# Kernel tuning notes

Measured on AMD Instinct MI355X. Metric: run time of the kernel, lower is better.

Reference implementation:

```python
import jax, jax.numpy as jnp
import numpy as np

IMG_W, IMG_H = 960.0, 512.0   # image_size (w, h)
HM_W, HM_H = 240, 128         # heatmap_size (w, h)


def _bilinear(fmap, gx, gy):
    # fmap: [C,H,W]; gx, gy: [N] normalized coords; bilinear, align_corners=False, zero padding
    C, H, W = fmap.shape
    ix = (gx + 1.0) * W * 0.5 - 0.5
    iy = (gy + 1.0) * H * 0.5 - 0.5
    x0f = jnp.floor(ix); y0f = jnp.floor(iy)
    wx1 = ix - x0f; wy1 = iy - y0f

    def tap(xf, yf, wgt):
        valid = (xf >= 0) & (xf <= W - 1) & (yf >= 0) & (yf <= H - 1)
        xc = jnp.clip(xf.astype(jnp.int32), 0, W - 1)
        yc = jnp.clip(yf.astype(jnp.int32), 0, H - 1)
        return fmap[:, yc, xc] * (wgt * valid.astype(fmap.dtype))

    return (tap(x0f, y0f, (1 - wx1) * (1 - wy1)) + tap(x0f + 1, y0f, wx1 * (1 - wy1))
            + tap(x0f, y0f + 1, (1 - wx1) * wy1) + tap(x0f + 1, y0f + 1, wx1 * wy1))


def _forward(feature_maps, grid_center, space_center, space_size, sub_space_size,
             cube, centers, trans, cam_R, cam_T, cam_f, cam_c):
    n_cam, B, C, H, W = feature_maps.shape
    vox = jnp.float32(cube)
    fine_n = (space_size / sub_space_size * (vox - 1.0)).astype(jnp.int32) + 1   # [3]
    fine_nf = fine_n.astype(jnp.float32)
    scale = (fine_nf - 1.0) / space_size
    bias = (-sub_space_size / 2.0 / space_size * (fine_nf - 1.0)
            - scale * (space_center - space_size / 2.0))
    centers_tl = jnp.round(grid_center[:, :3] * scale + bias).astype(jnp.int32)  # [B,3]
    offset = (centers_tl.astype(jnp.float32) / (fine_nf - 1.0) * space_size
              - space_size / 2.0 + sub_space_size / 2.0)                          # [B,3]
    mask_xy = jnp.maximum(((1.0 - grid_center[:, 5:7]) / 2.0 * (vox - 1.0)).astype(jnp.int32), 0)
    mask = jnp.concatenate([mask_xy, jnp.zeros((B, 1), jnp.int32)], axis=1)       # [B,3]
    start = jnp.maximum(centers_tl + mask, 0)
    end = jnp.minimum(centers_tl + cube - mask, fine_n)
    end = jnp.maximum(end, start + 1)

    # fixed-size sub-cube of fine-grid indices; out-of-window cells are masked to 0
    v = jnp.arange(cube)
    mesh = jnp.stack(jnp.meshgrid(v, v, v, indexing="ij"), axis=-1).reshape(-1, 3)  # [N,3]
    fidx = centers_tl[:, None, :] + mesh[None]                                       # [B,N,3]
    valid = jnp.all((fidx >= start[:, None, :]) & (fidx < end[:, None, :]), axis=-1)  # [B,N]
    valid = valid & (grid_center[:, 3:4] >= 0)
    world = (space_center - space_size / 2.0
             + fidx.astype(jnp.float32) / (fine_nf - 1.0) * space_size)              # [B,N,3]

    # pinhole world->pixel per (batch, camera)
    rel = world[:, None, :, :] - cam_T[:, :, None, :]                                # [B,K,N,3]
    Xc = jnp.einsum("bkij,bknj->bkni", cam_R, rel)
    xy = cam_f[:, :, None, :] * Xc[..., :2] / Xc[..., 2:3] + cam_c[:, :, None, :]    # [B,K,N,2]
    maxwh = jnp.max(centers * 2.0, axis=-1)[:, :, None, None]
    xy = jnp.clip(xy, -1.0, maxwh)
    xy = jnp.einsum("bkij,bknj->bkni", trans[..., :2], xy) + trans[:, :, None, :, 2]  # affine crop
    xy = xy * jnp.array([HM_W / IMG_W, HM_H / IMG_H], jnp.float32)
    g = jnp.clip(xy / jnp.array([HM_W - 1.0, HM_H - 1.0], jnp.float32) * 2.0 - 1.0, -1.1, 1.1)

    fm = jnp.transpose(feature_maps, (1, 0, 2, 3, 4))                                # [B,K,C,H,W]
    samp = jax.vmap(jax.vmap(_bilinear))(fm, g[..., 0], g[..., 1])                   # [B,K,C,N]
    samp = samp * valid[:, None, None, :].astype(samp.dtype)
    cubes = jnp.sum(samp, axis=1) / (n_cam + 1e-6)            # mean agg (bounding==1)
    cubes = jnp.clip(cubes, 0.0, 1.0).reshape(B, C, cube, cube, cube)
    return cubes, offset


def setup_inputs() -> dict:
    key = jax.random.key(0)
    ks = jax.random.split(key, 10)
    n_cam, B, C, H, W = 5, 4, 15, 128, 240
    feature_maps = jax.random.uniform(ks[0], (n_cam, B, C, H, W), jnp.float32)
    xy = jax.random.uniform(ks[1], (B, 2), minval=-3000.0, maxval=3000.0)
    z = jax.random.uniform(ks[2], (B, 1), minval=800.0, maxval=1200.0)
    flag = jnp.ones((B, 2), jnp.float32)  # cols 3 (validity >= 0) and 4
    m = jax.random.uniform(ks[3], (B, 2), minval=0.6, maxval=1.0)  # cols 5:7 mask fracs
    grid_center = jnp.concatenate([xy, z, flag, m], axis=1)        # [B,7]
    space_center = jnp.array([0.0, 0.0, 1000.0], jnp.float32)
    space_size = jnp.array([8000.0, 8000.0, 2000.0], jnp.float32)
    sub_space_size = jnp.array([2000.0, 2000.0, 2000.0], jnp.float32)
    centers = jnp.array([IMG_W / 2, IMG_H / 2], jnp.float32) + \
        jax.random.uniform(ks[4], (B, n_cam, 2), minval=-5.0, maxval=5.0)
    base = jnp.array([[1.0, 0.0, 0.0], [0.0, 1.0, 0.0]], jnp.float32)
    trans = base + 0.01 * jax.random.normal(ks[5], (B, n_cam, 2, 3), jnp.float32)
    cam_R = jnp.eye(3, dtype=jnp.float32) + 0.05 * jax.random.normal(ks[6], (B, n_cam, 3, 3), jnp.float32)
    t_xy = jax.random.uniform(ks[7], (B, n_cam, 2), minval=-500.0, maxval=500.0)
    cam_T = jnp.concatenate([t_xy, jnp.full((B, n_cam, 1), -6000.0, jnp.float32)], axis=-1)
    cam_f = jax.random.uniform(ks[8], (B, n_cam, 2), minval=500.0, maxval=700.0)
    cam_c = jnp.array([IMG_W / 2, IMG_H / 2], jnp.float32) + \
        jax.random.uniform(ks[9], (B, n_cam, 2), minval=-10.0, maxval=10.0)
    return {"feature_maps": feature_maps, "grid_center": grid_center,
            "space_center": space_center, "space_size": space_size,
            "sub_space_size": sub_space_size, "sub_cube_size": 64,
            "centers": centers, "trans": trans, "cam_R": cam_R,
            "cam_T": cam_T, "cam_f": cam_f, "cam_c": cam_c}


def reference(feature_maps, grid_center, space_center, space_size, sub_space_size,
              sub_cube_size, centers, trans, cam_R, cam_T, cam_f, cam_c):
    return _forward(feature_maps, grid_center, space_center, space_size, sub_space_size,
                    int(sub_cube_size), centers, trans, cam_R, cam_T, cam_f, cam_c)
```

## Files before the change

### kernel.cpp

```cpp
#include <hip/hip_runtime.h>
#include <hip/hip_fp16.h>

#define NCAM 5
#define NC 15
#define NCP 16
#define FH 128
#define FW 240
#define HW (FH*FW)
#define CUBE 64
#define NVOX (CUBE*CUBE*CUBE)
#define TTHREADS 256
#define MTHREADS 256
#define CSTR 24

__global__ __launch_bounds__(TTHREADS) void transpose_fm(
    const float* __restrict__ fm, __half* __restrict__ fmH,
    const float* __restrict__ gc, const float* __restrict__ space_c,
    const float* __restrict__ space_s, const float* __restrict__ sub_s,
    const float* __restrict__ centers, const float* __restrict__ trans,
    const float* __restrict__ cam_R, const float* __restrict__ cam_T,
    const float* __restrict__ cam_f, const float* __restrict__ cam_c,
    float* __restrict__ camS, int* __restrict__ bwin,
    float* __restrict__ out, int B)
{
    const int t = threadIdx.x;
    const int cb = blockIdx.y;
    const int cam = cb / B, b = cb - cam * B;
    const int bk = b * NCAM + cam;

    if (blockIdx.x == 0 && blockIdx.y == 0) {
        if (t < B) {
            const int bb = t;
            #pragma unroll
            for (int d = 0; d < 3; ++d) {
                float ssz = space_s[d], sc = space_c[d], sub = sub_s[d];
                int   fn  = (int)(ssz / sub * (CUBE - 1.0f)) + 1;
                float fnf = (float)fn;
                float scale = (fnf - 1.0f) / ssz;
                float bias  = -sub / 2.0f / ssz * (fnf - 1.0f) - scale * (sc - ssz / 2.0f);
                int ctl = (int)rintf(gc[bb*7 + d] * scale + bias);
                int mask = 0;
                if (d < 2) {
                    mask = (int)((1.0f - gc[bb*7 + 5 + d]) / 2.0f * (CUBE - 1.0f));
                    if (mask < 0) mask = 0;
                }
                int st = max(ctl + mask, 0);
                int en = min(ctl + CUBE - mask, fn);
                en = max(en, st + 1);
                bwin[bb*12 + d]     = ctl;
                bwin[bb*12 + 3 + d] = st;
                bwin[bb*12 + 6 + d] = en;
                out[(size_t)B * NC * NVOX + bb*3 + d] =
                    (float)ctl / (fnf - 1.0f) * ssz - ssz / 2.0f + sub / 2.0f;
            }
            bwin[t*12 + 9] = (gc[t*7 + 3] >= 0.0f) ? 1 : 0;
        }
        if (t < B * NCAM) {
            const int k = t;
            float sA[3], bA[3];
            #pragma unroll
            for (int d = 0; d < 3; ++d) {
                float ssz = space_s[d], sub = sub_s[d];
                int   fn  = (int)(ssz / sub * (CUBE - 1.0f)) + 1;
                sA[d] = ssz / ((float)fn - 1.0f);
                bA[d] = space_c[d] - ssz * 0.5f;
            }
            const float* R = cam_R + k*9;
            const float* T = cam_T + k*3;
            float* P = camS + (size_t)k * CSTR;
            #pragma unroll
            for (int i = 0; i < 3; ++i) {
                #pragma unroll
                for (int d = 0; d < 3; ++d) P[i*3 + d] = R[i*3 + d] * sA[d];
                P[9 + i] = R[i*3+0]*(bA[0]-T[0]) + R[i*3+1]*(bA[1]-T[1]) + R[i*3+2]*(bA[2]-T[2]);
            }
            P[12] = cam_f[k*2+0];  P[13] = cam_f[k*2+1];
            P[14] = cam_c[k*2+0];  P[15] = cam_c[k*2+1];
            P[16] = fmaxf(centers[k*2+0]*2.0f, centers[k*2+1]*2.0f);
            const float* tr = trans + k*6;
            const float KX = 60.0f/239.0f, KY = 32.0f/127.0f;
            P[17] = tr[0]*KX;  P[18] = tr[1]*KX;  P[19] = tr[2]*KX - 120.0f;
            P[20] = tr[3]*KY;  P[21] = tr[4]*KY;  P[22] = tr[5]*KY - 64.0f;
            P[23] = 0.0f;
        }
    }

    float sA[3], bA[3];
    #pragma unroll
    for (int d = 0; d < 3; ++d) {
        float ssz = space_s[d], sub = sub_s[d];
        int fn = (int)(ssz / sub * (CUBE - 1.0f)) + 1;
        sA[d] = ssz / ((float)fn - 1.0f);
        bA[d] = space_c[d] - ssz * 0.5f;
    }
    const float* R = cam_R + bk*9;
    const float* T = cam_T + bk*3;
    float M[9], tv[3];
    #pragma unroll
    for (int i = 0; i < 3; ++i) {
        #pragma unroll
        for (int d = 0; d < 3; ++d) M[i*3+d] = R[i*3+d] * sA[d];
        tv[i] = R[i*3+0]*(bA[0]-T[0]) + R[i*3+1]*(bA[1]-T[1]) + R[i*3+2]*(bA[2]-T[2]);
    }
    const float f0 = cam_f[bk*2+0], f1 = cam_f[bk*2+1];
    const float c0 = cam_c[bk*2+0], c1 = cam_c[bk*2+1];
    const float mw = fmaxf(centers[bk*2+0]*2.0f, centers[bk*2+1]*2.0f);
    const float* tr = trans + bk*6;
    const float KX = 60.0f/239.0f, KY = 32.0f/127.0f;
    const float ax = tr[0]*KX, bx_ = tr[1]*KX, cxo = tr[2]*KX - 120.0f;
    const float ay = tr[3]*KY, by_ = tr[4]*KY, cyo = tr[5]*KY - 64.0f;

    float ctlf[3];
    #pragma unroll
    for (int d = 0; d < 3; ++d) {
        float ssz = space_s[d], sc = space_c[d], sub = sub_s[d];
        int fn = (int)(ssz / sub * (CUBE - 1.0f)) + 1;
        float fnf = (float)fn;
        float scale = (fnf - 1.0f) / ssz;
        float bias = -sub/2.0f/ssz*(fnf-1.0f) - scale*(sc - ssz/2.0f);
        ctlf[d] = rintf(gc[b*7+d]*scale + bias);
    }

    float pxmin = 1e30f, pxmax = -1e30f, pymin = 1e30f, pymax = -1e30f;
    bool ok = true;
    #pragma unroll
    for (int ci = 0; ci < 8; ++ci) {
        float vx = ctlf[0] + ((ci & 1) ? 63.0f : 0.0f);
        float vy = ctlf[1] + ((ci & 2) ? 63.0f : 0.0f);
        float vz = ctlf[2] + ((ci & 4) ? 63.0f : 0.0f);
        float X0 = fmaf(M[0],vx, fmaf(M[1],vy, fmaf(M[2],vz, tv[0])));
        float X1 = fmaf(M[3],vx, fmaf(M[4],vy, fmaf(M[5],vz, tv[1])));
        float X2 = fmaf(M[6],vx, fmaf(M[7],vy, fmaf(M[8],vz, tv[2])));
        ok = ok && (X2 > 1e-3f);
        float rz = __builtin_amdgcn_rcpf(X2);
        float px = fmaf(f0*X0, rz, c0);
        float py = fmaf(f1*X1, rz, c1);
        pxmin = fminf(pxmin, px); pxmax = fmaxf(pxmax, px);
        pymin = fminf(pymin, py); pymax = fmaxf(pymax, py);
    }
    int bbx0, bbx1, bby0, bby1;
    if (ok) {
        float pxl = fminf(fmaxf(pxmin,-1.0f),mw), pxh = fminf(fmaxf(pxmax,-1.0f),mw);
        float pyl = fminf(fmaxf(pymin,-1.0f),mw), pyh = fminf(fmaxf(pymax,-1.0f),mw);
        float ixlo = (ax>0.f?ax*pxl:ax*pxh) + (bx_>0.f?bx_*pyl:bx_*pyh) + cxo;
        float ixhi = (ax>0.f?ax*pxh:ax*pxl) + (bx_>0.f?bx_*pyh:bx_*pyl) + cxo;
        ixlo = fminf(fmaxf(ixlo,-132.0f),132.0f) + 119.5f;
        ixhi = fminf(fmaxf(ixhi,-132.0f),132.0f) + 119.5f;
        float iylo = (ay>0.f?ay*pxl:ay*pxh) + (by_>0.f?by_*pyl:by_*pyh) + cyo;
        float iyhi = (ay>0.f?ay*pxh:ay*pxl) + (by_>0.f?by_*pyh:by_*pyl) + cyo;
        iylo = fminf(fmaxf(iylo,-70.4f),70.4f) + 63.5f;
        iyhi = fminf(fmaxf(iyhi,-70.4f),70.4f) + 63.5f;
        bbx0 = max((int)floorf(ixlo) - 1, 0);
        bbx1 = min((int)floorf(ixhi) + 2, FW-1);
        bby0 = max((int)floorf(iylo) - 1, 0);
        bby1 = min((int)floorf(iyhi) + 2, FH-1);
    } else {
        bbx0 = 0; bbx1 = FW-1; bby0 = 0; bby1 = FH-1;
    }

    const int p0  = blockIdx.x * TTHREADS;
    const int rlo = p0 / FW, rhi = (p0 + TTHREADS - 1) / FW;
    if (rhi < bby0 || rlo > bby1) return;
    const int p   = p0 + t;
    const int pyy = p / FW, pxx = p - pyy * FW;
    if (pyy < bby0 || pyy > bby1 || pxx < bbx0 || pxx > bbx1) return;

    const float* src = fm + (size_t)cb * NC * HW + p;
    __half v[NCP];
    #pragma unroll
    for (int c = 0; c < NC; ++c) v[c] = __float2half(src[(size_t)c * HW]);
    v[15] = __float2half(0.0f);
    uint4* dst = (uint4*)(fmH + ((size_t)cb * HW + p) * NCP);
    dst[0] = *(const uint4*)(v);
    dst[1] = *(const uint4*)(v + 8);
}

__device__ __forceinline__ __half2 u2h(unsigned u) {
    __half2 h; __builtin_memcpy(&h, &u, 4); return h;
}

#define TAPFMA2(W2, A, Bv)                                                    \
    acc2[0] = __hfma2((W2), u2h(A.x),  acc2[0]);                              \
    acc2[1] = __hfma2((W2), u2h(A.y),  acc2[1]);                              \
    acc2[2] = __hfma2((W2), u2h(A.z),  acc2[2]);                              \
    acc2[3] = __hfma2((W2), u2h(A.w),  acc2[3]);                              \
    acc2[4] = __hfma2((W2), u2h(Bv.x), acc2[4]);                              \
    acc2[5] = __hfma2((W2), u2h(Bv.y), acc2[5]);                              \
    acc2[6] = __hfma2((W2), u2h(Bv.z), acc2[6]);                              \
    acc2[7] = __hfma2((W2), u2h(Bv.w), acc2[7]);

__global__ __launch_bounds__(MTHREADS) void proj_main(
    const __half* __restrict__ fmH,
    const float* __restrict__ camS,
    const int* __restrict__ bwin,
    float* __restrict__ out, int B)
{
    const unsigned nwg = gridDim.x;
    const unsigned q = nwg >> 3, r = nwg & 7;
    const unsigned xcd = blockIdx.x & 7, idx = blockIdx.x >> 3;
    const unsigned wgid = (xcd < r ? xcd * (q + 1) : r * (q + 1) + (xcd - r) * q) + idx;

    const int b = wgid >> 10;
    const int n = (int)(wgid & 1023) * MTHREADS + threadIdx.x;
    const int vi = n >> 12, vj = (n >> 6) & 63, vk = n & 63;

    const int* W = bwin + b*12;
    const int fx = W[0] + vi, fy = W[1] + vj, fz = W[2] + vk;
    const bool valid = (fx >= W[3]) & (fx < W[6])
                     & (fy >= W[4]) & (fy < W[7])
                     & (fz >= W[5]) & (fz < W[8])
                     & (W[9] != 0);

    __half2 acc2[8];
    #pragma unroll
    for (int i = 0; i < 8; ++i) acc2[i] = __half2half2(__float2half(0.0f));

    if (valid) {
        const float fxf = (float)fx, fyf = (float)fy, fzf = (float)fz;
        const float* cs = camS + (size_t)(b * NCAM) * CSTR;

        #pragma unroll
        for (int cam = 0; cam < NCAM; ++cam) {
            const float* P = cs + cam * CSTR;
            float X0 = fmaf(P[0], fxf, fmaf(P[1], fyf, fmaf(P[2], fzf, P[9])));
            float X1 = fmaf(P[3], fxf, fmaf(P[4], fyf, fmaf(P[5], fzf, P[10])));
            float X2 = fmaf(P[6], fxf, fmaf(P[7], fyf, fmaf(P[8], fzf, P[11])));
            float rz = __builtin_amdgcn_rcpf(X2);
            float px = fmaf(P[12]*X0, rz, P[14]);
            float py = fmaf(P[13]*X1, rz, P[15]);
            float mw = P[16];
            px = fminf(fmaxf(px, -1.0f), mw);
            py = fminf(fmaxf(py, -1.0f), mw);
            float ixf = fminf(fmaxf(fmaf(P[17], px, fmaf(P[18], py, P[19])), -132.0f), 132.0f) + 119.5f;
            float iyf = fminf(fmaxf(fmaf(P[20], px, fmaf(P[21], py, P[22])), -70.4f), 70.4f) + 63.5f;
            float x0f = floorf(ixf), y0f = floorf(iyf);
            float wx1 = ixf - x0f,  wy1 = iyf - y0f;
            float wx0 = 1.0f - wx1, wy0 = 1.0f - wy1;
            int x0 = (int)x0f, y0 = (int)y0f, x1 = x0 + 1, y1 = y0 + 1;
            bool vx0 = (unsigned)x0 <= (FW-1), vx1 = (unsigned)x1 <= (FW-1);
            bool vy0 = (unsigned)y0 <= (FH-1), vy1 = (unsigned)y1 <= (FH-1);
            float w0 = (vx0 && vy0) ? wx0*wy0 : 0.0f;
            float w1 = (vx1 && vy0) ? wx1*wy0 : 0.0f;
            float w2 = (vx0 && vy1) ? wx0*wy1 : 0.0f;
            float w3 = (vx1 && vy1) ? wx1*wy1 : 0.0f;
            int xc0 = min(max(x0,0),FW-1), xc1 = min(max(x1,0),FW-1);
            int yc0 = min(max(y0,0),FH-1), yc1 = min(max(y1,0),FH-1);

            const __half* bp  = fmH + (size_t)(cam*B + b) * HW * NCP;
            const __half* t00 = bp  + (size_t)(yc0*FW + xc0) * NCP;
            const __half* t10 = t00 + (size_t)(xc1 - xc0) * NCP;
            const __half* t01 = t00 + (size_t)(yc1 - yc0) * (FW * NCP);
            const __half* t11 = t01 + (size_t)(xc1 - xc0) * NCP;

            uint4 a0 = ((const uint4*)t00)[0], b0 = ((const uint4*)t00)[1];
            uint4 a1 = ((const uint4*)t10)[0], b1 = ((const uint4*)t10)[1];
            uint4 a2 = ((const uint4*)t01)[0], b2 = ((const uint4*)t01)[1];
            uint4 a3 = ((const uint4*)t11)[0], b3 = ((const uint4*)t11)[1];

            __half2 w20 = __float2half2_rn(w0);
            __half2 w21 = __float2half2_rn(w1);
            __half2 w22 = __float2half2_rn(w2);
            __half2 w23 = __float2half2_rn(w3);

            TAPFMA2(w20, a0, b0)
            TAPFMA2(w21, a1, b1)
            TAPFMA2(w22, a2, b2)
            TAPFMA2(w23, a3, b3)
        }
    }

    const float RINV = 0.19999996000000800f;
    #pragma unroll
    for (int i = 0; i < 8; ++i) {
        float2 f = __half22float2(acc2[i]);
        int c0i = 2*i, c1i = 2*i + 1;
        float v0 = fminf(fmaxf(f.x * RINV, 0.0f), 1.0f);
        out[((size_t)(b*NC + c0i)) * NVOX + n] = v0;
        if (c1i < NC) {
            float v1 = fminf(fmaxf(f.y * RINV, 0.0f), 1.0f);
            out[((size_t)(b*NC + c1i)) * NVOX + n] = v1;
        }
    }
}

__global__ __launch_bounds__(256) void proj_fallback(
    const float* __restrict__ fm, const float* __restrict__ gc,
    const float* __restrict__ space_center, const float* __restrict__ space_size,
    const float* __restrict__ sub_size, const float* __restrict__ centers,
    const float* __restrict__ trans, const float* __restrict__ cam_R,
    const float* __restrict__ cam_T, const float* __restrict__ cam_f,
    const float* __restrict__ cam_c, float* __restrict__ out, int B)
{
    const int b = blockIdx.x / (NVOX/256);
    const int n = (blockIdx.x % (NVOX/256)) * 256 + threadIdx.x;
    float ctlf[3], fnf[3], sc[3], ssz[3];
    int   ctl[3], st[3], en[3];
    #pragma unroll
    for (int d = 0; d < 3; ++d) {
        ssz[d] = space_size[d];
        sc[d]  = space_center[d];
        float sub = sub_size[d];
        int fn = (int)(ssz[d] / sub * (CUBE - 1.0f)) + 1;
        fnf[d] = (float)fn;
        float scale = (fnf[d] - 1.0f) / ssz[d];
        float bias  = -sub / 2.0f / ssz[d] * (fnf[d] - 1.0f)
                      - scale * (sc[d] - ssz[d] / 2.0f);
        int c_tl = (int)rintf(gc[b*7 + d] * scale + bias);
        ctl[d]  = c_tl;  ctlf[d] = (float)c_tl;
        int mask = 0;
        if (d < 2) {
            mask = (int)((1.0f - gc[b*7 + 5 + d]) / 2.0f * (CUBE - 1.0f));
            if (mask < 0) mask = 0;
        }
        st[d] = max(c_tl + mask, 0);
        int e = min(c_tl + CUBE - mask, fn);
        en[d] = max(e, st[d] + 1);
    }
    if (n < 3) {
        int d = n;
        out[(size_t)B * NC * NVOX + b*3 + d] =
            ctlf[d] / (fnf[d] - 1.0f) * ssz[d] - ssz[d] / 2.0f + sub_size[d] / 2.0f;
    }
    const int vi = n >> 12, vj = (n >> 6) & 63, vk = n & 63;
    const int fx = ctl[0] + vi, fy = ctl[1] + vj, fz = ctl[2] + vk;
    const bool valid = (fx >= st[0]) & (fx < en[0]) & (fy >= st[1]) & (fy < en[1])
                     & (fz >= st[2]) & (fz < en[2]) & (gc[b*7 + 3] >= 0.0f);
    float acc[NC];
    #pragma unroll
    for (int c = 0; c < NC; ++c) acc[c] = 0.0f;
    if (valid) {
        const float wxw = sc[0] - ssz[0]*0.5f + (float)fx / (fnf[0]-1.0f) * ssz[0];
        const float wyw = sc[1] - ssz[1]*0.5f + (float)fy / (fnf[1]-1.0f) * ssz[1];
        const float wzw = sc[2] - ssz[2]*0.5f + (float)fz / (fnf[2]-1.0f) * ssz[2];
        for (int cam = 0; cam < NCAM; ++cam) {
            const int bk = b*NCAM + cam;
            const float* R = cam_R + bk*9;
            const float* T = cam_T + bk*3;
            float r0 = wxw - T[0], r1 = wyw - T[1], r2 = wzw - T[2];
            float X0 = R[0]*r0 + R[1]*r1 + R[2]*r2;
            float X1 = R[3]*r0 + R[4]*r1 + R[5]*r2;
            float X2 = R[6]*r0 + R[7]*r1 + R[8]*r2;
            float px = cam_f[bk*2+0]*X0/X2 + cam_c[bk*2+0];
            float py = cam_f[bk*2+1]*X1/X2 + cam_c[bk*2+1];
            float maxwh = fmaxf(centers[bk*2+0]*2.0f, centers[bk*2+1]*2.0f);
            px = fminf(fmaxf(px, -1.0f), maxwh);
            py = fminf(fmaxf(py, -1.0f), maxwh);
            const float* tr = trans + bk*6;
            float tx = (tr[0]*px + tr[1]*py + tr[2]) * 0.25f;
            float ty = (tr[3]*px + tr[4]*py + tr[5]) * 0.25f;
            float gx = fminf(fmaxf(tx/239.0f*2.0f - 1.0f, -1.1f), 1.1f);
            float gy = fminf(fmaxf(ty/127.0f*2.0f - 1.0f, -1.1f), 1.1f);
            float ixf = (gx + 1.0f)*(FW*0.5f) - 0.5f;
            float iyf = (gy + 1.0f)*(FH*0.5f) - 0.5f;
            float x0f = floorf(ixf), y0f = floorf(iyf);
            float wx1 = ixf - x0f,  wy1 = iyf - y0f;
            float wx0 = 1.0f - wx1, wy0 = 1.0f - wy1;
            int x0 = (int)x0f, y0 = (int)y0f, x1 = x0 + 1, y1 = y0 + 1;
            bool vx0 = (x0 >= 0) & (x0 <= FW-1), vx1 = (x1 >= 0) & (x1 <= FW-1);
            bool vy0 = (y0 >= 0) & (y0 <= FH-1), vy1 = (y1 >= 0) & (y1 <= FH-1);
            float w00 = wx0*wy0*(float)(vx0 & vy0);
            float w10 = wx1*wy0*(float)(vx1 & vy0);
            float w01 = wx0*wy1*(float)(vx0 & vy1);
            float w11 = wx1*wy1*(float)(vx1 & vy1);
            int xc0 = min(max(x0,0),FW-1), xc1 = min(max(x1,0),FW-1);
            int yc0 = min(max(y0,0),FH-1), yc1 = min(max(y1,0),FH-1);
            int o00 = yc0*FW + xc0, o10 = yc0*FW + xc1;
            int o01 = yc1*FW + xc0, o11 = yc1*FW + xc1;
            const float* base = fm + ((size_t)(cam*B + b)) * NC * HW;
            #pragma unroll
            for (int c = 0; c < NC; ++c) {
                const float* p = base + c*HW;
                acc[c] += w00*p[o00] + w10*p[o10] + w01*p[o01] + w11*p[o11];
            }
        }
    }
    const float invd = (float)(5.0 + 1e-6);
    #pragma unroll
    for (int c = 0; c < NC; ++c) {
        float v = acc[c] / invd;
        v = fminf(fmaxf(v, 0.0f), 1.0f);
        out[((size_t)(b*NC + c)) * NVOX + n] = v;
    }
}

extern "C" void kernel_launch(void* const* d_in, const int* in_sizes, int n_in,
                              void* d_out, int out_size, void* d_ws, size_t ws_size,
                              hipStream_t stream) {
    const float* fm        = (const float*)d_in[0];
    const float* gc        = (const float*)d_in[1];
    const float* space_c   = (const float*)d_in[2];
    const float* space_s   = (const float*)d_in[3];
    const float* sub_s     = (const float*)d_in[4];
    const float* centers   = (const float*)d_in[6];
    const float* trans     = (const float*)d_in[7];
    const float* cam_R     = (const float*)d_in[8];
    const float* cam_T     = (const float*)d_in[9];
    const float* cam_f     = (const float*)d_in[10];
    const float* cam_c     = (const float*)d_in[11];
    float* out = (float*)d_out;
    const int B = in_sizes[1] / 7;

    const size_t FMHB   = (size_t)NCAM * B * HW * NCP * sizeof(__half);
    const size_t CAMOFF = (FMHB + 255) & ~(size_t)255;
    const size_t BWOFF  = (CAMOFF + (size_t)B * NCAM * CSTR * 4 + 255) & ~(size_t)255;
    const size_t NEED   = BWOFF + (size_t)B * 48;

    if (ws_size >= NEED) {
        __half* fmH  = (__half*)d_ws;
        float*  camS = (float*)((char*)d_ws + CAMOFF);
        int*    bwin = (int*)((char*)d_ws + BWOFF);
        dim3 tg(HW / TTHREADS, NCAM * B);
        hipLaunchKernelGGL(transpose_fm, tg, dim3(TTHREADS), 0, stream,
                           fm, fmH, gc, space_c, space_s, sub_s, centers, trans,
                           cam_R, cam_T, cam_f, cam_c, camS, bwin, out, B);
        dim3 grid(B * 1024), block(MTHREADS);
        hipLaunchKernelGGL(proj_main, grid, block, 0, stream,
                           fmH, camS, bwin, out, B);
    } else {
        dim3 grid(B * (NVOX/256)), block(256);
        hipLaunchKernelGGL(proj_fallback, grid, block, 0, stream,
                           fm, gc, space_c, space_s, sub_s,
                           centers, trans, cam_R, cam_T, cam_f, cam_c, out, B);
    }
}
```

Baseline: 40.30 us.

## Process two adjacent-y voxels per thread in projection kernel

Each thread now handles two voxels that differ by one in y, so the grid is halved and the per-thread x/z validity checks and camera parameter loads are shared between them. The two sets of bilinear gathers are issued back to back to raise memory-level parallelism per thread. Launch bounds are also tightened to request four waves' worth of occupancy. The cost is higher register pressure from two accumulator sets and eight in-flight tap loads per camera, and fewer threads in total.

```diff
diff --git a/kernel.cpp b/kernel.cpp
--- a/kernel.cpp
+++ b/kernel.cpp
@@ -179,17 +179,50 @@
     __half2 h; __builtin_memcpy(&h, &u, 4); return h;
 }
 
-#define TAPFMA2(W2, A, Bv)                                                    \
-    acc2[0] = __hfma2((W2), u2h(A.x),  acc2[0]);                              \
-    acc2[1] = __hfma2((W2), u2h(A.y),  acc2[1]);                              \
-    acc2[2] = __hfma2((W2), u2h(A.z),  acc2[2]);                              \
-    acc2[3] = __hfma2((W2), u2h(A.w),  acc2[3]);                              \
-    acc2[4] = __hfma2((W2), u2h(Bv.x), acc2[4]);                              \
-    acc2[5] = __hfma2((W2), u2h(Bv.y), acc2[5]);                              \
-    acc2[6] = __hfma2((W2), u2h(Bv.z), acc2[6]);                              \
-    acc2[7] = __hfma2((W2), u2h(Bv.w), acc2[7]);
-
-__global__ __launch_bounds__(MTHREADS) void proj_main(
+#define TAPFMA2(ACC, W2, A, Bv)                                               \
+    ACC[0] = __hfma2((W2), u2h(A.x),  ACC[0]);                                \
+    ACC[1] = __hfma2((W2), u2h(A.y),  ACC[1]);                                \
+    ACC[2] = __hfma2((W2), u2h(A.z),  ACC[2]);                                \
+    ACC[3] = __hfma2((W2), u2h(A.w),  ACC[3]);                                \
+    ACC[4] = __hfma2((W2), u2h(Bv.x), ACC[4]);                                \
+    ACC[5] = __hfma2((W2), u2h(Bv.y), ACC[5]);                                \
+    ACC[6] = __hfma2((W2), u2h(Bv.z), ACC[6]);                                \
+    ACC[7] = __hfma2((W2), u2h(Bv.w), ACC[7]);
+
+#define PROJ_TAPS(P, FYF, VF, W20, W21, W22, W23, T00, T10, T01, T11)         \
+    {                                                                         \
+        float X0 = fmaf(P[0], fxf, fmaf(P[1], (FYF), fmaf(P[2], fzf, P[9]))); \
+        float X1 = fmaf(P[3], fxf, fmaf(P[4], (FYF), fmaf(P[5], fzf, P[10])));\
+        float X2 = fmaf(P[6], fxf, fmaf(P[7], (FYF), fmaf(P[8], fzf, P[11])));\
+        float rz = __builtin_amdgcn_rcpf(X2);                                 \
+        float px = fmaf(P[12]*X0, rz, P[14]);                                 \
+        float py = fmaf(P[13]*X1, rz, P[15]);                                 \
+        float mw = P[16];                                                     \
+        px = fminf(fmaxf(px, -1.0f), mw);                                     \
+        py = fminf(fmaxf(py, -1.0f), mw);                                     \
+        float ixf = fminf(fmaxf(fmaf(P[17], px, fmaf(P[18], py, P[19])), -132.0f), 132.0f) + 119.5f; \
+        float iyf = fminf(fmaxf(fmaf(P[20], px, fmaf(P[21], py, P[22])), -70.4f), 70.4f) + 63.5f;    \
+        float x0f = floorf(ixf), y0f = floorf(iyf);                           \
+        float wx1 = ixf - x0f,  wy1 = iyf - y0f;                              \
+        float wx0 = 1.0f - wx1, wy0 = 1.0f - wy1;                             \
+        int x0 = (int)x0f, y0 = (int)y0f, x1 = x0 + 1, y1 = y0 + 1;           \
+        bool vx0 = (unsigned)x0 <= (FW-1), vx1 = (unsigned)x1 <= (FW-1);      \
+        bool vy0 = (unsigned)y0 <= (FH-1), vy1 = (unsigned)y1 <= (FH-1);      \
+        float w0 = ((vx0 && vy0) ? wx0*wy0 : 0.0f) * (VF);                    \
+        float w1 = ((vx1 && vy0) ? wx1*wy0 : 0.0f) * (VF);                    \
+        float w2 = ((vx0 && vy1) ? wx0*wy1 : 0.0f) * (VF);                    \
+        float w3 = ((vx1 && vy1) ? wx1*wy1 : 0.0f) * (VF);                    \
+        W20 = __float2half2_rn(w0);  W21 = __float2half2_rn(w1);              \
+        W22 = __float2half2_rn(w2);  W23 = __float2half2_rn(w3);              \
+        int xc0 = min(max(x0,0),FW-1), xc1 = min(max(x1,0),FW-1);             \
+        int yc0 = min(max(y0,0),FH-1), yc1 = min(max(y1,0),FH-1);             \
+        T00 = bp  + (size_t)(yc0*FW + xc0) * NCP;                             \
+        T10 = T00 + (size_t)(xc1 - xc0) * NCP;                                \
+        T01 = T00 + (size_t)(yc1 - yc0) * (FW * NCP);                         \
+        T11 = T01 + (size_t)(xc1 - xc0) * NCP;                                \
+    }
+
+__global__ __launch_bounds__(MTHREADS, 4) void proj_main(
     const __half* __restrict__ fmH,
     const float* __restrict__ camS,
     const int* __restrict__ bwin,
@@ -200,85 +233,81 @@
     const unsigned xcd = blockIdx.x & 7, idx = blockIdx.x >> 3;
     const unsigned wgid = (xcd < r ? xcd * (q + 1) : r * (q + 1) + (xcd - r) * q) + idx;
 
-    const int b = wgid >> 10;
-    const int n = (int)(wgid & 1023) * MTHREADS + threadIdx.x;
-    const int vi = n >> 12, vj = (n >> 6) & 63, vk = n & 63;
+    const int b = wgid >> 9;
+    const int t = threadIdx.x;
+    const int n0 = (int)(wgid & 511) * 512 + (t >> 6) * 128 + (t & 63);
+    const int n1 = n0 + 64;
+    const int vi = n0 >> 12, vj0 = (n0 >> 6) & 63, vk = n0 & 63;
 
     const int* W = bwin + b*12;
-    const int fx = W[0] + vi, fy = W[1] + vj, fz = W[2] + vk;
-    const bool valid = (fx >= W[3]) & (fx < W[6])
-                     & (fy >= W[4]) & (fy < W[7])
-                     & (fz >= W[5]) & (fz < W[8])
-                     & (W[9] != 0);
-
-    __half2 acc2[8];
-    #pragma unroll
-    for (int i = 0; i < 8; ++i) acc2[i] = __half2half2(__float2half(0.0f));
-
-    if (valid) {
-        const float fxf = (float)fx, fyf = (float)fy, fzf = (float)fz;
+    const int fx = W[0] + vi, fz = W[2] + vk;
+    const int fy0 = W[1] + vj0, fy1 = fy0 + 1;
+    const bool okxz = (fx >= W[3]) & (fx < W[6])
+                    & (fz >= W[5]) & (fz < W[8])
+                    & (W[9] != 0);
+    const bool valid0 = okxz & (fy0 >= W[4]) & (fy0 < W[7]);
+    const bool valid1 = okxz & (fy1 >= W[4]) & (fy1 < W[7]);
+
+    __half2 accA[8], accB[8];
+    #pragma unroll
+    for (int i = 0; i < 8; ++i) {
+        accA[i] = __half2half2(__float2half(0.0f));
+        accB[i] = __half2half2(__float2half(0.0f));
+    }
+
+    if (valid0 | valid1) {
+        const float fxf = (float)fx, fzf = (float)fz;
+        const float fyf0 = (float)fy0, fyf1 = (float)fy1;
+        const float vf0 = valid0 ? 1.0f : 0.0f;
+        const float vf1 = valid1 ? 1.0f : 0.0f;
         const float* cs = camS + (size_t)(b * NCAM) * CSTR;
 
         #pragma unroll
         for (int cam = 0; cam < NCAM; ++cam) {
             const float* P = cs + cam * CSTR;
-            float X0 = fmaf(P[0], fxf, fmaf(P[1], fyf, fmaf(P[2], fzf, P[9])));
-            float X1 = fmaf(P[3], fxf, fmaf(P[4], fyf, fmaf(P[5], fzf, P[10])));
-            float X2 = fmaf(P[6], fxf, fmaf(P[7], fyf, fmaf(P[8], fzf, P[11])));
-            float rz = __builtin_amdgcn_rcpf(X2);
-            float px = fmaf(P[12]*X0, rz, P[14]);
-            float py = fmaf(P[13]*X1, rz, P[15]);
-            float mw = P[16];
-            px = fminf(fmaxf(px, -1.0f), mw);
-            py = fminf(fmaxf(py, -1.0f), mw);
-            float ixf = fminf(fmaxf(fmaf(P[17], px, fmaf(P[18], py, P[19])), -132.0f), 132.0f) + 119.5f;
-            float iyf = fminf(fmaxf(fmaf(P[20], px, fmaf(P[21], py, P[22])), -70.4f), 70.4f) + 63.5f;
-            float x0f = floorf(ixf), y0f = floorf(iyf);
-            float wx1 = ixf - x0f,  wy1 = iyf - y0f;
-            float wx0 = 1.0f - wx1, wy0 = 1.0f - wy1;
-            int x0 = (int)x0f, y0 = (int)y0f, x1 = x0 + 1, y1 = y0 + 1;
-            bool vx0 = (unsigned)x0 <= (FW-1), vx1 = (unsigned)x1 <= (FW-1);
-            bool vy0 = (unsigned)y0 <= (FH-1), vy1 = (unsigned)y1 <= (FH-1);
-            float w0 = (vx0 && vy0) ? wx0*wy0 : 0.0f;
-            float w1 = (vx1 && vy0) ? wx1*wy0 : 0.0f;
-            float w2 = (vx0 && vy1) ? wx0*wy1 : 0.0f;
-            float w3 = (vx1 && vy1) ? wx1*wy1 : 0.0f;
-            int xc0 = min(max(x0,0),FW-1), xc1 = min(max(x1,0),FW-1);
-            int yc0 = min(max(y0,0),FH-1), yc1 = min(max(y1,0),FH-1);
-
-            const __half* bp  = fmH + (size_t)(cam*B + b) * HW * NCP;
-            const __half* t00 = bp  + (size_t)(yc0*FW + xc0) * NCP;
-            const __half* t10 = t00 + (size_t)(xc1 - xc0) * NCP;
-            const __half* t01 = t00 + (size_t)(yc1 - yc0) * (FW * NCP);
-            const __half* t11 = t01 + (size_t)(xc1 - xc0) * NCP;
-
-            uint4 a0 = ((const uint4*)t00)[0], b0 = ((const uint4*)t00)[1];
-            uint4 a1 = ((const uint4*)t10)[0], b1 = ((const uint4*)t10)[1];
-            uint4 a2 = ((const uint4*)t01)[0], b2 = ((const uint4*)t01)[1];
-            uint4 a3 = ((const uint4*)t11)[0], b3 = ((const uint4*)t11)[1];
-
-            __half2 w20 = __float2half2_rn(w0);
-            __half2 w21 = __float2half2_rn(w1);
-            __half2 w22 = __float2half2_rn(w2);
-            __half2 w23 = __float2half2_rn(w3);
-
-            TAPFMA2(w20, a0, b0)
-            TAPFMA2(w21, a1, b1)
-            TAPFMA2(w22, a2, b2)
-            TAPFMA2(w23, a3, b3)
+            const __half* bp = fmH + (size_t)(cam*B + b) * HW * NCP;
+
+            __half2 wA0, wA1, wA2, wA3, wB0, wB1, wB2, wB3;
+            const __half *tA00, *tA10, *tA01, *tA11;
+            const __half *tB00, *tB10, *tB01, *tB11;
+
+            PROJ_TAPS(P, fyf0, vf0, wA0, wA1, wA2, wA3, tA00, tA10, tA01, tA11)
+            uint4 aA0 = ((const uint4*)tA00)[0], bA0 = ((const uint4*)tA00)[1];
+            uint4 aA1 = ((const uint4*)tA10)[0], bA1 = ((const uint4*)tA10)[1];
+            uint4 aA2 = ((const uint4*)tA01)[0], bA2 = ((const uint4*)tA01)[1];
+            uint4 aA3 = ((const uint4*)tA11)[0], bA3 = ((const uint4*)tA11)[1];
+
+            PROJ_TAPS(P, fyf1, vf1, wB0, wB1, wB2, wB3, tB00, tB10, tB01, tB11)
+            uint4 aB0 = ((const uint4*)tB00)[0], bB0 = ((const uint4*)tB00)[1];
+            uint4 aB1 = ((const uint4*)tB10)[0], bB1 = ((const uint4*)tB10)[1];
+            uint4 aB2 = ((const uint4*)tB01)[0], bB2 = ((const uint4*)tB01)[1];
+            uint4 aB3 = ((const uint4*)tB11)[0], bB3 = ((const uint4*)tB11)[1];
+
+            TAPFMA2(accA, wA0, aA0, bA0)
+            TAPFMA2(accA, wA1, aA1, bA1)
+            TAPFMA2(accA, wA2, aA2, bA2)
+            TAPFMA2(accA, wA3, aA3, bA3)
+
+            TAPFMA2(accB, wB0, aB0, bB0)
+            TAPFMA2(accB, wB1, aB1, bB1)
+            TAPFMA2(accB, wB2, aB2, bB2)
+            TAPFMA2(accB, wB3, aB3, bB3)
         }
     }
 
     const float RINV = 0.19999996000000800f;
     #pragma unroll
     for (int i = 0; i < 8; ++i) {
-        float2 f = __half22float2(acc2[i]);
+        float2 fA = __half22float2(accA[i]);
+        float2 fB = __half22float2(accB[i]);
         int c0i = 2*i, c1i = 2*i + 1;
-        float v0 = fminf(fmaxf(f.x * RINV, 0.0f), 1.0f);
-        out[((size_t)(b*NC + c0i)) * NVOX + n] = v0;
+        const size_t base0 = ((size_t)(b*NC + c0i)) * NVOX;
+        out[base0 + n0] = fminf(fmaxf(fA.x * RINV, 0.0f), 1.0f);
+        out[base0 + n1] = fminf(fmaxf(fB.x * RINV, 0.0f), 1.0f);
         if (c1i < NC) {
-            float v1 = fminf(fmaxf(f.y * RINV, 0.0f), 1.0f);
-            out[((size_t)(b*NC + c1i)) * NVOX + n] = v1;
+            const size_t base1 = ((size_t)(b*NC + c1i)) * NVOX;
+            out[base1 + n0] = fminf(fmaxf(fA.y * RINV, 0.0f), 1.0f);
+            out[base1 + n1] = fminf(fmaxf(fB.y * RINV, 0.0f), 1.0f);
         }
     }
 }
@@ -413,7 +442,7 @@
         hipLaunchKernelGGL(transpose_fm, tg, dim3(TTHREADS), 0, stream,
                            fm, fmH, gc, space_c, space_s, sub_s, centers, trans,
                            cam_R, cam_T, cam_f, cam_c, camS, bwin, out, B);
-        dim3 grid(B * 1024), block(MTHREADS);
+        dim3 grid(B * 512), block(MTHREADS);
         hipLaunchKernelGGL(proj_main, grid, block, 0, stream,
                            fmH, camS, bwin, out, B);
     } else {
```

New measurement: 45.39 us. 1.13x slower.
